# Kernel tuning notes

Hardware: AMD Instinct MI355X
Metric: run time of the kernel (lower is better)

The kernel has to match this reference:

```python
import jax, jax.numpy as jnp
import numpy as np

B, N, C, P = 16, 4096, 4, 64
D = 128        # conv output channels (fixed in module)
WIN = 7        # window_size
ALPHA = 0.5
EPS = 1e-5     # BatchNorm eps


def setup_inputs() -> dict:
    key = jax.random.key(0)
    k1, k2, k3, k4 = jax.random.split(key, 4)
    x = jax.random.normal(k1, (B, N, C, P), jnp.float32)
    x_template = jax.random.normal(k2, (B, N, C, P), jnp.float32)
    # Conv1d(n_channel, 128, kernel_size=n_pts): weight [128, C, P], bias [128]
    W = jax.random.normal(k3, (D, C, P), jnp.float32) * 0.05
    b = jax.random.normal(k4, (D,), jnp.float32) * 0.01
    gamma = jnp.ones((D,), jnp.float32)   # BN weight init = 1
    beta = jnp.zeros((D,), jnp.float32)   # BN bias init = 0
    return {"x": x, "x_template": x_template, "W": W, "b": b, "gamma": gamma, "beta": beta}


def _embed(x_flat, W, b, gamma, beta):
    # Conv1d with kernel_size == full length -> contraction over (C, P), output length 1.
    h = jnp.einsum('ncp,dcp->nd', x_flat, W) + b           # [B*N, D]
    # BatchNorm1d in training mode: per-channel stats over the (B*N, L=1) batch.
    mean = h.mean(axis=0)
    var = h.var(axis=0)                                     # biased variance (torch BN)
    h = (h - mean) / jnp.sqrt(var + EPS) * gamma + beta
    return jnp.where(h >= 0, h, 0.1 * h)                    # LeakyReLU(0.1)


def reference(x, x_template, W, b, gamma, beta):
    nb, nc, ch, npt = x.shape
    hw = WIN // 2
    off = jnp.arange(-hw, hw + 1)
    raw = jnp.arange(nc)[:, None] + off[None, :]
    valid = (raw >= 0) & (raw < nc)                         # dedups clamped edge cols (matches dense mask)
    cols = jnp.clip(raw, 0, nc - 1)

    emb_x = _embed(x.reshape(nb * nc, ch, npt), W, b, gamma, beta).reshape(nb, nc, D)
    emb_t = _embed(x_template.reshape(nb * nc, ch, npt), W, b, gamma, beta).reshape(nb, nc, D)

    # Banded similarity: only the window entries the module actually uses.
    emb_t_win = emb_t[:, cols]
    sim = jnp.einsum('bnd,bnwd->bnw', emb_x, emb_t_win)

    # feat_fused = raw sim gathered at clamped window inds (duplicates at edges kept)
    feat_fused = sim

    # Masked softmax over the window (invalid = clamped duplicates excluded, as in dense mask)
    mx = jnp.where(valid, sim, -jnp.inf).max(axis=-1, keepdims=True)
    e = jnp.where(valid, jnp.exp(sim - mx), 0.0)
    attn = e / e.sum(axis=-1, keepdims=True)

    xt_flat = x_template.reshape(nb, nc, ch * npt)
    out = jnp.einsum('bnw,bnwe->bne', attn, xt_flat[:, cols])  # [B, N, C*P]
    out = out.reshape(nb, nc, ch, npt)
    out = ALPHA * x + (1.0 - ALPHA) * out
    return out, feat_fused
```

## Files before the change

kernel.cpp:

```cpp
#include <hip/hip_runtime.h>
#include <math.h>

#define BB 16
#define NN 4096
#define DD 128
#define KK 256
#define NROWS (BB*NN)
#define WIN 7
#define HWIN 3
#define ALPHA 0.5f
#define EPS 1e-5f

typedef __attribute__((ext_vector_type(8))) short bf16x8;
typedef __attribute__((ext_vector_type(4))) float f32x4;

__device__ __forceinline__ unsigned short f2b(float f) {
    unsigned u = __float_as_uint(f);
    u += 0x7FFFu + ((u >> 16) & 1u);
    return (unsigned short)(u >> 16);
}
__device__ __forceinline__ float b2f_lo(unsigned v) { return __uint_as_float(v << 16); }
__device__ __forceinline__ float b2f_hi(unsigned v) { return __uint_as_float(v & 0xFFFF0000u); }
__device__ __forceinline__ float lrelu(float v) { return v >= 0.f ? v : 0.1f * v; }

__device__ __forceinline__ unsigned cvtpk(float lo, float hi) {
    unsigned r;
    asm("v_cvt_pk_bf16_f32 %0, %1, %2" : "=v"(r) : "v"(lo), "v"(hi));
    return r;
}

__device__ __forceinline__ uint4 pack8(float4 a, float4 b) {
    uint4 v;
    v.x = (unsigned)f2b(a.x)  | ((unsigned)f2b(a.y)  << 16);
    v.y = (unsigned)f2b(a.z)  | ((unsigned)f2b(a.w)  << 16);
    v.z = (unsigned)f2b(b.x)  | ((unsigned)f2b(b.y)  << 16);
    v.w = (unsigned)f2b(b.z)  | ((unsigned)f2b(b.w)  << 16);
    return v;
}

#define GL2LDS(gp, lp) __builtin_amdgcn_global_load_lds( \
    (const __attribute__((address_space(1))) void*)(gp), \
    (__attribute__((address_space(3))) void*)(lp), 16, 0, 0)

__global__ __launch_bounds__(256) void k_prep(
    const float* __restrict__ W, uint4* __restrict__ Wfrag)
{
    const int id   = blockIdx.x * 256 + threadIdx.x;
    const int lane = id & 63, f = id >> 6;
    const int k = f & 7, w = f >> 3;
    const int d = w * 16 + (lane & 15);
    const int c = k * 32 + (lane >> 4) * 8;
    const float4 a = *(const float4*)(&W[(size_t)d * KK + c]);
    const float4 b = *(const float4*)(&W[(size_t)d * KK + c + 4]);
    Wfrag[id] = pack8(a, b);
}

__global__ __launch_bounds__(512, 4) void k_embed(
    const float* __restrict__ x,
    const float* __restrict__ xt,
    const uint4* __restrict__ Wfrag,
    const float* __restrict__ bvec,
    unsigned short* __restrict__ h_out,
    float* __restrict__ sums)
{
    __shared__ float Xs[2][32 * 256];

    const int blk  = blockIdx.x;
    const int src  = blk >> 8;
    const int tile = blk & 255;
    const int row0 = tile * 256;
    const float* __restrict__ X = src ? xt : x;
    unsigned short* __restrict__ H = h_out + (size_t)src * NROWS * DD;

    const int t    = threadIdx.x;
    const int lane = t & 63;
    const int w    = t >> 6;
    const int l15  = lane & 15;
    const int lg   = lane >> 4;

    bf16x8 breg[8];
    #pragma unroll
    for (int k = 0; k < 8; ++k) {
        uint4 u = Wfrag[(w * 8 + k) * 64 + lane];
        breg[k] = *(bf16x8*)&u;
    }

    const float bv = bvec[w * 16 + l15];
    float s = 0.f, q = 0.f;

    #define STAGE(sub, b)                                                     \
    {                                                                         \
        const float* base_ = X + (size_t)(row0 + (sub) * 32) * KK;            \
        _Pragma("unroll")                                                     \
        for (int j_ = 0; j_ < 4; ++j_) {                                      \
            const int i_ = w * 4 + j_;                                        \
            const float* gp_ = base_ + i_ * KK + ((lane ^ (i_ & 15)) << 2);   \
            GL2LDS(gp_, &Xs[b][i_ * 256]);                                    \
        }                                                                     \
    }

    STAGE(0, 0);
    __syncthreads();

    #pragma unroll 1
    for (int st = 0; st < 8; ++st) {
        if (st < 7) STAGE(st + 1, (st + 1) & 1);

        const float* xb = &Xs[st & 1][0];
        f32x4 acc[2];
        #pragma unroll
        for (int m = 0; m < 2; ++m)
            #pragma unroll
            for (int j = 0; j < 4; ++j) acc[m][j] = 0.f;

        #pragma unroll
        for (int k = 0; k < 8; ++k) {
            const int u0 = k * 8 + lg * 2;
            #pragma unroll
            for (int m = 0; m < 2; ++m) {
                const float* pr = xb + (m * 16 + l15) * 256;
                const f32x4 a0 = *(const f32x4*)(pr + ((u0 ^ l15) << 2));
                const f32x4 a1 = *(const f32x4*)(pr + (((u0 + 1) ^ l15) << 2));
                uint4 uu;
                uu.x = cvtpk(a0[0], a0[1]);
                uu.y = cvtpk(a0[2], a0[3]);
                uu.z = cvtpk(a1[0], a1[1]);
                uu.w = cvtpk(a1[2], a1[3]);
                const bf16x8 av = *(const bf16x8*)&uu;
                acc[m] = __builtin_amdgcn_mfma_f32_16x16x32_bf16(av, breg[k], acc[m], 0, 0, 0);
            }
        }

        #pragma unroll
        for (int m = 0; m < 2; ++m) {
            #pragma unroll
            for (int j = 0; j < 4; ++j) {
                const int row = row0 + st * 32 + m * 16 + lg * 4 + j;
                const float v = acc[m][j] + bv;
                H[(size_t)row * DD + w * 16 + l15] = f2b(v);
                s += v; q += v * v;
            }
        }
        __syncthreads();
    }

    s += __shfl_xor(s, 16); s += __shfl_xor(s, 32);
    q += __shfl_xor(q, 16); q += __shfl_xor(q, 32);
    if (lane < 16) {
        atomicAdd(&sums[src * 256 + w * 16 + l15], s);
        atomicAdd(&sums[src * 256 + 128 + w * 16 + l15], q);
    }
    #undef STAGE
}

__global__ __launch_bounds__(256) void k_attn(
    const float* __restrict__ x,
    const float* __restrict__ xt,
    const unsigned short* __restrict__ h,
    const float* __restrict__ sums,
    const float* __restrict__ gamma,
    const float* __restrict__ beta,
    float* __restrict__ out,
    float* __restrict__ feat)
{
    const int blk  = blockIdx.x;
    const int bb   = blk >> 7;
    const int tile = blk & 127;
    const int n0   = tile * 32;
    const int t    = threadIdx.x;

    __shared__ float ex[32][132];
    __shared__ float et[38][132];
    __shared__ float attnw[32][8];
    __shared__ float ssl[512];

    const unsigned short* __restrict__ Hx = h;
    const unsigned short* __restrict__ Ht = h + (size_t)NROWS * DD;
    const size_t rowbase = (size_t)bb * NN;

    {
        const int s_ = t >> 7, d = t & 127;
        const float invn = 1.0f / (float)NROWS;
        const float mean = sums[s_ * 256 + d] * invn;
        const float var  = sums[s_ * 256 + 128 + d] * invn - mean * mean;
        const float sc   = gamma[d] / sqrtf(var + EPS);
        ssl[s_ * 256 + d]       = sc;
        ssl[s_ * 256 + 128 + d] = beta[d] - mean * sc;
    }
    __syncthreads();

    #pragma unroll
    for (int p = 0; p < 2; ++p) {
        const int j = t + p * 256;
        const int r = j >> 4, c8 = j & 15;
        const uint4 u = *(const uint4*)(&Hx[(rowbase + n0 + r) * DD + c8 * 8]);
        const float4 sca = *(const float4*)(&ssl[c8 * 8]);
        const float4 scb = *(const float4*)(&ssl[c8 * 8 + 4]);
        const float4 sha = *(const float4*)(&ssl[128 + c8 * 8]);
        const float4 shb = *(const float4*)(&ssl[128 + c8 * 8 + 4]);
        float* dst = &ex[r][c8 * 8];
        dst[0] = lrelu(b2f_lo(u.x) * sca.x + sha.x);
        dst[1] = lrelu(b2f_hi(u.x) * sca.y + sha.y);
        dst[2] = lrelu(b2f_lo(u.y) * sca.z + sha.z);
        dst[3] = lrelu(b2f_hi(u.y) * sca.w + sha.w);
        dst[4] = lrelu(b2f_lo(u.z) * scb.x + shb.x);
        dst[5] = lrelu(b2f_hi(u.z) * scb.y + shb.y);
        dst[6] = lrelu(b2f_lo(u.w) * scb.z + shb.z);
        dst[7] = lrelu(b2f_hi(u.w) * scb.w + shb.w);
    }
    #pragma unroll
    for (int p = 0; p < 3; ++p) {
        const int j = t + p * 256;
        if (j < 608) {
            const int r = j >> 4, c8 = j & 15;
            int g = n0 - HWIN + r;
            g = min(max(g, 0), NN - 1);
            const uint4 u = *(const uint4*)(&Ht[(rowbase + g) * DD + c8 * 8]);
            const float4 sca = *(const float4*)(&ssl[256 + c8 * 8]);
            const float4 scb = *(const float4*)(&ssl[256 + c8 * 8 + 4]);
            const float4 sha = *(const float4*)(&ssl[384 + c8 * 8]);
            const float4 shb = *(const float4*)(&ssl[384 + c8 * 8 + 4]);
            float* dst = &et[r][c8 * 8];
            dst[0] = lrelu(b2f_lo(u.x) * sca.x + sha.x);
            dst[1] = lrelu(b2f_hi(u.x) * sca.y + sha.y);
            dst[2] = lrelu(b2f_lo(u.y) * sca.z + sha.z);
            dst[3] = lrelu(b2f_hi(u.y) * sca.w + sha.w);
            dst[4] = lrelu(b2f_lo(u.z) * scb.x + shb.x);
            dst[5] = lrelu(b2f_hi(u.z) * scb.y + shb.y);
            dst[6] = lrelu(b2f_lo(u.w) * scb.z + shb.z);
            dst[7] = lrelu(b2f_hi(u.w) * scb.w + shb.w);
        }
    }
    __syncthreads();

    if (t < 224) {
        const int n_i = t / 7;
        const int wv  = t % 7;
        const float* a = &ex[n_i][0];
        const float* b = &et[n_i + wv][0];
        float acc = 0.f;
        #pragma unroll
        for (int d4 = 0; d4 < 128; d4 += 4) {
            const float4 av = *(const float4*)(a + d4);
            const float4 bv = *(const float4*)(b + d4);
            acc += av.x * bv.x + av.y * bv.y + av.z * bv.z + av.w * bv.w;
        }
        feat[(rowbase + n0 + n_i) * WIN + wv] = acc;
        attnw[n_i][wv] = acc;
    }
    __syncthreads();

    unsigned short* xts = (unsigned short*)&et[0][0];
    if (t < 224) {
        #pragma unroll
        for (int p = 0; p < 6; ++p) {
            const int j = t + p * 224;
            if (j < 1216) {
                const int r = j >> 5, c8 = j & 31;
                int g = n0 - HWIN + r;
                g = min(max(g, 0), NN - 1);
                const float* gp = &xt[(rowbase + g) * KK + c8 * 8];
                const float4 a = *(const float4*)(gp);
                const float4 b = *(const float4*)(gp + 4);
                *(uint4*)((char*)xts + r * 512 + c8 * 16) = pack8(a, b);
            }
        }
    } else {
        const int n_i = t - 224;
        const int n = n0 + n_i;
        float mx = -1e30f;
        #pragma unroll
        for (int wv = 0; wv < WIN; ++wv) {
            const int c = n + wv - HWIN;
            if (c >= 0 && c < NN) mx = fmaxf(mx, attnw[n_i][wv]);
        }
        float e[WIN];
        float esum = 0.f;
        #pragma unroll
        for (int wv = 0; wv < WIN; ++wv) {
            const int c = n + wv - HWIN;
            const bool valid = (c >= 0 && c < NN);
            e[wv] = valid ? expf(attnw[n_i][wv] - mx) : 0.f;
            esum += e[wv];
        }
        const float inv = 1.0f / esum;
        #pragma unroll
        for (int wv = 0; wv < WIN; ++wv) attnw[n_i][wv] = e[wv] * inv;
    }
    __syncthreads();

    #pragma unroll
    for (int p = 0; p < 8; ++p) {
        const int idx = t + p * 256;
        const int n_i = idx >> 6, e4 = idx & 63;
        const int n = n0 + n_i;
        const float4 xv = *(const float4*)(&x[(rowbase + n) * KK + e4 * 4]);
        float4 acc = make_float4(0.f, 0.f, 0.f, 0.f);
        #pragma unroll
        for (int wv = 0; wv < WIN; ++wv) {
            const float aw = attnw[n_i][wv];
            const uint2 u = *(const uint2*)((const char*)xts + (n_i + wv) * 512 + e4 * 8);
            acc.x += aw * b2f_lo(u.x);
            acc.y += aw * b2f_hi(u.x);
            acc.z += aw * b2f_lo(u.y);
            acc.w += aw * b2f_hi(u.y);
        }
        float4 o;
        o.x = ALPHA * xv.x + (1.f - ALPHA) * acc.x;
        o.y = ALPHA * xv.y + (1.f - ALPHA) * acc.y;
        o.z = ALPHA * xv.z + (1.f - ALPHA) * acc.z;
        o.w = ALPHA * xv.w + (1.f - ALPHA) * acc.w;
        *(float4*)(&out[(rowbase + n) * KK + e4 * 4]) = o;
    }
}

extern "C" void kernel_launch(void* const* d_in, const int* in_sizes, int n_in,
                              void* d_out, int out_size, void* d_ws, size_t ws_size,
                              hipStream_t stream) {
    const float* x     = (const float*)d_in[0];
    const float* xt    = (const float*)d_in[1];
    const float* W     = (const float*)d_in[2];
    const float* bvec  = (const float*)d_in[3];
    const float* gamma = (const float*)d_in[4];
    const float* beta  = (const float*)d_in[5];

    float* out  = (float*)d_out;
    float* feat = out + (size_t)BB * NN * KK;

    char* ws = (char*)d_ws;
    unsigned short* h  = (unsigned short*)ws;
    float* sums        = (float*)(ws + 33554432);
    unsigned char* Wfr = (unsigned char*)(ws + 33556480);

    hipMemsetAsync(sums, 0, 512 * sizeof(float), stream);
    k_prep<<<16, 256, 0, stream>>>(W, (uint4*)Wfr);
    k_embed<<<512, 512, 0, stream>>>(x, xt, (const uint4*)Wfr, bvec, h, sums);
    k_attn<<<2048, 256, 0, stream>>>(x, xt, h, sums, gamma, beta, out, feat);
}
```

Measured before the change: 218.9 us.

## Split attention kernel into similarity/softmax and output-mixing kernels

Splits the fused attention kernel into two. k_sim computes the similarities and softmax weights and writes them to a workspace. k_out reads the weights and does the windowed weighted sum directly from global fp32 x_template, with a swizzled block order, instead of staging a bf16 copy in shared memory. This removes the shared-memory staging and the bf16 rounding, and lets each kernel use resources independently. In exchange it adds a kernel launch, a small attention-weight round trip through global memory, and seven overlapping global reads per output element that rely on cache hits.

Result: slower. 229.5 us (+4.8%).

```diff
diff --git a/kernel.cpp b/kernel.cpp
--- a/kernel.cpp
+++ b/kernel.cpp
@@ -143,6 +143,7 @@
         }
         __syncthreads();
     }
+    #undef STAGE
 
     s += __shfl_xor(s, 16); s += __shfl_xor(s, 32);
     q += __shfl_xor(q, 16); q += __shfl_xor(q, 32);
@@ -150,17 +151,14 @@
         atomicAdd(&sums[src * 256 + w * 16 + l15], s);
         atomicAdd(&sums[src * 256 + 128 + w * 16 + l15], q);
     }
-    #undef STAGE
-}
-
-__global__ __launch_bounds__(256) void k_attn(
-    const float* __restrict__ x,
-    const float* __restrict__ xt,
+}
+
+__global__ __launch_bounds__(256) void k_sim(
     const unsigned short* __restrict__ h,
     const float* __restrict__ sums,
     const float* __restrict__ gamma,
     const float* __restrict__ beta,
-    float* __restrict__ out,
+    float* __restrict__ attn_ws,
     float* __restrict__ feat)
 {
     const int blk  = blockIdx.x;
@@ -250,29 +248,13 @@
     }
     __syncthreads();
 
-    unsigned short* xts = (unsigned short*)&et[0][0];
-    if (t < 224) {
-        #pragma unroll
-        for (int p = 0; p < 6; ++p) {
-            const int j = t + p * 224;
-            if (j < 1216) {
-                const int r = j >> 5, c8 = j & 31;
-                int g = n0 - HWIN + r;
-                g = min(max(g, 0), NN - 1);
-                const float* gp = &xt[(rowbase + g) * KK + c8 * 8];
-                const float4 a = *(const float4*)(gp);
-                const float4 b = *(const float4*)(gp + 4);
-                *(uint4*)((char*)xts + r * 512 + c8 * 16) = pack8(a, b);
-            }
-        }
-    } else {
-        const int n_i = t - 224;
-        const int n = n0 + n_i;
+    if (t < 32) {
+        const int n = n0 + t;
         float mx = -1e30f;
         #pragma unroll
         for (int wv = 0; wv < WIN; ++wv) {
             const int c = n + wv - HWIN;
-            if (c >= 0 && c < NN) mx = fmaxf(mx, attnw[n_i][wv]);
+            if (c >= 0 && c < NN) mx = fmaxf(mx, attnw[t][wv]);
         }
         float e[WIN];
         float esum = 0.f;
@@ -280,15 +262,37 @@
         for (int wv = 0; wv < WIN; ++wv) {
             const int c = n + wv - HWIN;
             const bool valid = (c >= 0 && c < NN);
-            e[wv] = valid ? expf(attnw[n_i][wv] - mx) : 0.f;
+            e[wv] = valid ? expf(attnw[t][wv] - mx) : 0.f;
             esum += e[wv];
         }
         const float inv = 1.0f / esum;
         #pragma unroll
-        for (int wv = 0; wv < WIN; ++wv) attnw[n_i][wv] = e[wv] * inv;
-    }
-    __syncthreads();
-
+        for (int wv = 0; wv < WIN; ++wv) attnw[t][wv] = e[wv] * inv;
+        attnw[t][7] = 0.f;
+    }
+    __syncthreads();
+
+    attn_ws[(size_t)blk * 256 + t] = attnw[t >> 3][t & 7];
+}
+
+__global__ __launch_bounds__(256) void k_out(
+    const float* __restrict__ x,
+    const float* __restrict__ xt,
+    const float* __restrict__ attn_ws,
+    float* __restrict__ out)
+{
+    const int braw = blockIdx.x;
+    const int blk  = (braw & 7) * 256 + (braw >> 3);
+    const int bb   = blk >> 7;
+    const int tile = blk & 127;
+    const int n0   = tile * 32;
+    const int t    = threadIdx.x;
+
+    __shared__ float als[256];
+    als[t] = attn_ws[(size_t)blk * 256 + t];
+    __syncthreads();
+
+    const size_t rowbase = (size_t)bb * NN;
     #pragma unroll
     for (int p = 0; p < 8; ++p) {
         const int idx = t + p * 256;
@@ -298,12 +302,14 @@
         float4 acc = make_float4(0.f, 0.f, 0.f, 0.f);
         #pragma unroll
         for (int wv = 0; wv < WIN; ++wv) {
-            const float aw = attnw[n_i][wv];
-            const uint2 u = *(const uint2*)((const char*)xts + (n_i + wv) * 512 + e4 * 8);
-            acc.x += aw * b2f_lo(u.x);
-            acc.y += aw * b2f_hi(u.x);
-            acc.z += aw * b2f_lo(u.y);
-            acc.w += aw * b2f_hi(u.y);
+            int g = n + wv - HWIN;
+            g = min(max(g, 0), NN - 1);
+            const float aw = als[n_i * 8 + wv];
+            const float4 tv = *(const float4*)(&xt[(rowbase + g) * KK + e4 * 4]);
+            acc.x += aw * tv.x;
+            acc.y += aw * tv.y;
+            acc.z += aw * tv.z;
+            acc.w += aw * tv.w;
         }
         float4 o;
         o.x = ALPHA * xv.x + (1.f - ALPHA) * acc.x;
@@ -331,9 +337,11 @@
     unsigned short* h  = (unsigned short*)ws;
     float* sums        = (float*)(ws + 33554432);
     unsigned char* Wfr = (unsigned char*)(ws + 33556480);
+    float* attn        = (float*)(ws + 33622016);
 
     hipMemsetAsync(sums, 0, 512 * sizeof(float), stream);
     k_prep<<<16, 256, 0, stream>>>(W, (uint4*)Wfr);
     k_embed<<<512, 512, 0, stream>>>(x, xt, (const uint4*)Wfr, bvec, h, sums);
-    k_attn<<<2048, 256, 0, stream>>>(x, xt, h, sums, gamma, beta, out, feat);
-}
+    k_sim<<<2048, 256, 0, stream>>>(h, sums, gamma, beta, attn, feat);
+    k_out<<<2048, 256, 0, stream>>>(x, xt, attn, out);
+}
```
